# Kernel tuning notes

Hardware: AMD Instinct MI355X
Metric: run time of the kernel (lower is better)

The kernel has to match this reference:

```python
import jax, jax.numpy as jnp
import numpy as np
from jax import lax

B, C, T = 8, 512, 2048
TEMP = 0.07
EPS = 1e-12


def setup_inputs() -> dict:
    key = jax.random.key(0)
    k1, k2, k3, k4 = jax.random.split(key, 4)
    x = jax.random.normal(k1, (B, C, T), dtype=jnp.float32)
    w_qkv = jax.random.normal(k2, (3 * C, C, 1), dtype=jnp.float32) * (1.0 / np.sqrt(C))
    w_dw = jax.random.normal(k3, (3 * C, 1, 3), dtype=jnp.float32) * (1.0 / np.sqrt(3))
    w_proj = jax.random.normal(k4, (C, C, 1), dtype=jnp.float32) * (1.0 / np.sqrt(C))
    return {"x": x, "w_qkv": w_qkv, "w_dw": w_dw, "w_proj": w_proj}


def _l2norm_ch(a):
    # F.normalize(a, dim=1): divide by L2 norm over channel dim, clamped at eps
    n = jnp.sqrt(jnp.sum(a * a, axis=1, keepdims=True))
    return a / jnp.maximum(n, EPS)


def reference(x, w_qkv, w_dw, w_proj):
    # 1x1 conv: [B,C,T] x [3C,C] -> [B,3C,T]
    qkv = jnp.einsum('bct,oc->bot', x, w_qkv[:, :, 0])
    # depthwise conv, kernel 3, padding 1, groups = 3C
    qkv = lax.conv_general_dilated(
        qkv, w_dw, window_strides=(1,), padding=[(1, 1)],
        dimension_numbers=('NCH', 'OIH', 'NCH'), feature_group_count=3 * C)
    q, k, v = jnp.split(qkv, 3, axis=1)  # each [B,C,T]
    q = _l2norm_ch(q)
    k = _l2norm_ch(k)
    # attn over tokens: [B,T,T]
    attn = jax.nn.softmax(jnp.einsum('bct,bcs->bts', q, k) / TEMP, axis=-1)
    out = jnp.einsum('bts,bcs->bct', attn, v)  # [B,C,T]
    return jnp.einsum('bct,oc->bot', out, w_proj[:, :, 0])
```

## Files before the change

### kernel.cpp

```cpp
#include <hip/hip_runtime.h>
#include <math.h>

static constexpr int B_ = 8, C_ = 512, T_ = 2048, C3_ = 1536;
static constexpr float INV_TEMP = 1.0f / 0.07f;

typedef __attribute__((ext_vector_type(8))) short short8;
typedef __attribute__((ext_vector_type(4))) float floatx4;

__device__ __forceinline__ float b2f(unsigned short u) {
  union { unsigned int i; float f; } v; v.i = ((unsigned int)u) << 16; return v.f;
}
__device__ __forceinline__ unsigned short f2b(float f) {
  union { float f; unsigned int i; } v; v.f = f;
  const unsigned int x = v.i;
  return (unsigned short)((x + 0x7FFFu + ((x >> 16) & 1u)) >> 16);
}
__device__ __forceinline__ void gld16(const unsigned short* g, unsigned short* l) {
  __builtin_amdgcn_global_load_lds(
      (const __attribute__((address_space(1))) void*)g,
      (__attribute__((address_space(3))) void*)l, 16, 0, 0);
}

#define FENCE  asm volatile("" ::: "memory")
#define BAR()  do { FENCE; __builtin_amdgcn_s_barrier(); FENCE; } while (0)
#define LGKM0  asm volatile("s_waitcnt lgkmcnt(0)" ::: "memory")
#define VMC4   asm volatile("s_waitcnt vmcnt(4)" ::: "memory")
#define VMC0   asm volatile("s_waitcnt vmcnt(0)" ::: "memory")

template<bool OUT_BF16, int MODE>
__global__ __launch_bounds__(512, 2)
void gemm256(const unsigned short* __restrict__ A, const unsigned short* __restrict__ B,
             void* __restrict__ Cout, int K, int lda, int ldb, int ldc,
             long long sA, long long sB, long long sC,
             const float* __restrict__ rs, const float* __restrict__ cs,
             float* __restrict__ denom, int rcStride, float scale)
{
  extern __shared__ unsigned short S[];

  const int bz = blockIdx.z;
  A += (long long)bz * sA;
  B += (long long)bz * sB;
  if (MODE == 2) { rs += (long long)bz * rcStride; cs += (long long)bz * rcStride;
                   denom += (long long)bz * rcStride; }
  if (MODE == 3) { rs += (long long)bz * rcStride; }
  const int m0 = blockIdx.y * 256, n0 = blockIdx.x * 256;
  const int tid = threadIdx.x;
  const int w = tid >> 6, lane = tid & 63;
  const int rl = lane & 15, qd = lane >> 4;
  const int wm = (w >> 2) * 128, wn = (w & 3) * 64;

  const int lr = lane >> 3;
  const int lg = ((lane & 7) ^ lr) * 8;
  const unsigned short* gA = A + (long long)(m0 + w * 8 + lr) * lda + lg;
  const unsigned short* gB = B + (long long)(n0 + w * 8 + lr) * ldb + lg;

  const int g0 = (qd ^ (rl & 7)) * 8;
  const int g1 = ((4 + qd) ^ (rl & 7)) * 8;
  const int aBase = (wm + rl) * 64, bBase = (wn + rl) * 64;

  floatx4 acc[8][4];
  #pragma unroll
  for (int i = 0; i < 8; ++i)
    #pragma unroll
    for (int j = 0; j < 4; ++j) acc[i][j] = 0.0f;

  auto stA = [&](int buf, int h, int kt) {
    unsigned short* d = S + buf * 32768 + h * 8192 + w * 512;
    const unsigned short* s = gA + (long long)(h * 128) * lda + kt * 64;
    gld16(s, d);
    gld16(s + (long long)64 * lda, d + 4096);
  };
  auto stB = [&](int buf, int h, int kt) {
    unsigned short* d = S + buf * 32768 + 16384 + h * 8192 + w * 512;
    const unsigned short* s = gB + (long long)(h * 128) * ldb + kt * 64;
    gld16(s, d);
    gld16(s + (long long)64 * ldb, d + 4096);
  };

  short8 fa[4][2], fl[2][2], fr[2][2];
  auto rdA = [&](int buf, int ih) {
    const unsigned short* p = S + buf * 32768 + aBase + ih * 4096;
    #pragma unroll
    for (int i = 0; i < 4; ++i) {
      fa[i][0] = *(const short8*)(p + i * 1024 + g0);
      fa[i][1] = *(const short8*)(p + i * 1024 + g1);
    }
  };
  auto rdB = [&](short8 (&fb)[2][2], int buf, int jh) {
    const unsigned short* p = S + buf * 32768 + 16384 + bBase + jh * 2048;
    #pragma unroll
    for (int j = 0; j < 2; ++j) {
      fb[j][0] = *(const short8*)(p + j * 1024 + g0);
      fb[j][1] = *(const short8*)(p + j * 1024 + g1);
    }
  };
  auto mm = [&](short8 (&fb)[2][2], int ih, int jh) {
    #pragma unroll
    for (int i = 0; i < 4; ++i)
      #pragma unroll
      for (int j = 0; j < 2; ++j) {
        floatx4& a = acc[ih * 4 + i][jh * 2 + j];
        a = __builtin_amdgcn_mfma_f32_16x16x32_bf16(fa[i][0], fb[j][0], a, 0, 0, 0);
        a = __builtin_amdgcn_mfma_f32_16x16x32_bf16(fa[i][1], fb[j][1], a, 0, 0, 0);
      }
  };

  auto iter = [&](int kt, bool st2, bool st3, bool tail) {
    rdA(0, 0); rdB(fl, 0, 0);
    stA(1, 0, kt + 1);
    BAR(); LGKM0;
    __builtin_amdgcn_s_setprio(1); mm(fl, 0, 0); __builtin_amdgcn_s_setprio(0);
    BAR();
    rdB(fr, 0, 1);
    stA(1, 1, kt + 1);
    BAR(); LGKM0;
    __builtin_amdgcn_s_setprio(1); mm(fr, 0, 1); __builtin_amdgcn_s_setprio(0);
    BAR();
    rdA(0, 1);
    if (st2) stB(0, 0, kt + 2);
    BAR(); LGKM0;
    __builtin_amdgcn_s_setprio(1); mm(fl, 1, 0); __builtin_amdgcn_s_setprio(0);
    BAR();
    if (st2) stB(0, 1, kt + 2);
    if (tail) { VMC0; } else { VMC4; }
    BAR();
    __builtin_amdgcn_s_setprio(1); mm(fr, 1, 1); __builtin_amdgcn_s_setprio(0);
    BAR();
    rdA(1, 0); rdB(fl, 1, 0);
    if (st2) stA(0, 0, kt + 2);
    BAR(); LGKM0;
    __builtin_amdgcn_s_setprio(1); mm(fl, 0, 0); __builtin_amdgcn_s_setprio(0);
    BAR();
    rdB(fr, 1, 1);
    if (st2) stA(0, 1, kt + 2);
    BAR(); LGKM0;
    __builtin_amdgcn_s_setprio(1); mm(fr, 0, 1); __builtin_amdgcn_s_setprio(0);
    BAR();
    rdA(1, 1);
    if (st3) stB(1, 0, kt + 3);
    BAR(); LGKM0;
    __builtin_amdgcn_s_setprio(1); mm(fl, 1, 0); __builtin_amdgcn_s_setprio(0);
    BAR();
    if (st3) stB(1, 1, kt + 3);
    if (!tail) { VMC4; }
    BAR();
    __builtin_amdgcn_s_setprio(1); mm(fr, 1, 1); __builtin_amdgcn_s_setprio(0);
    BAR();
  };

  const int niter = K >> 7;
  stB(0, 0, 0); stB(0, 1, 0); stA(0, 0, 0); stA(0, 1, 0);
  stB(1, 0, 1); stB(1, 1, 1);
  VMC4; BAR();
  for (int i = 0; i < niter - 1; ++i) iter(2 * i, true, true, false);
  iter(2 * (niter - 1), false, false, true);

  float cf4[4];
  if (MODE == 2) {
    #pragma unroll
    for (int j = 0; j < 4; ++j) cf4[j] = cs[n0 + wn + j * 16 + rl];
  }
  #pragma unroll
  for (int i = 0; i < 8; ++i) {
    #pragma unroll
    for (int r = 0; r < 4; ++r) {
      const int row = m0 + wm + i * 16 + qd * 4 + r;
      float rowf = 0.f;
      if (MODE == 2) rowf = rs[row] * scale;
      if (MODE == 3) rowf = 1.0f / rs[row];
      float rsum = 0.f;
      #pragma unroll
      for (int j = 0; j < 4; ++j) {
        const int col = n0 + wn + j * 16 + rl;
        float v = acc[i][j][r];
        if (MODE == 2) {
          const float s = v * rowf * cf4[j];
          const unsigned short pb = f2b(__expf(s - scale));
          rsum += b2f(pb);
          ((unsigned short*)Cout)[(long long)bz * sC + (long long)row * ldc + col] = pb;
          continue;
        }
        if (MODE == 3) v *= rowf;
        const long long idx = (long long)bz * sC + (long long)row * ldc + col;
        if (OUT_BF16) ((unsigned short*)Cout)[idx] = f2b(v);
        else          ((float*)Cout)[idx] = v;
      }
      if (MODE == 2) {
        #pragma unroll
        for (int m = 1; m < 16; m <<= 1) rsum += __shfl_xor(rsum, m);
        if (rl == 0) atomicAdd(denom + row, rsum);
      }
    }
  }
}

__global__ __launch_bounds__(256)
void zero_f(float* __restrict__ p, int n)
{
  const int i = blockIdx.x * 256 + threadIdx.x;
  if (i < n) p[i] = 0.f;
}

__global__ __launch_bounds__(256)
void conv_xT(const float* __restrict__ x, unsigned short* __restrict__ xT)
{
  const int b = blockIdx.z, t0 = blockIdx.x * 32, c0 = blockIdx.y * 32;
  const int tx = threadIdx.x & 31, ty = threadIdx.x >> 5;
  __shared__ float tile[32][33];
  const float* src = x + (long long)b * C_ * T_;
  #pragma unroll
  for (int r = 0; r < 4; ++r)
    tile[ty + 8 * r][tx] = src[(long long)(c0 + ty + 8 * r) * T_ + t0 + tx];
  __syncthreads();
  unsigned short* dst = xT + (long long)b * T_ * C_;
  #pragma unroll
  for (int r = 0; r < 4; ++r)
    dst[(long long)(t0 + ty + 8 * r) * C_ + c0 + tx] = f2b(tile[tx][ty + 8 * r]);
}

__global__ __launch_bounds__(256)
void conv_bf(const float* __restrict__ in, unsigned short* __restrict__ out, int n)
{
  const int i = blockIdx.x * 256 + threadIdx.x;
  if (i < n) out[i] = f2b(in[i]);
}

__global__ __launch_bounds__(256)
void dw_v(const unsigned short* __restrict__ qkv, const float* __restrict__ wdw,
          unsigned short* __restrict__ vout)
{
  const long long idx = (long long)blockIdx.x * 256 + threadIdx.x;
  const int t = (int)(idx % T_);
  const long long rem = idx / T_;
  const int c = (int)(rem % C_), b = (int)(rem / C_);
  const unsigned short* src = qkv + ((long long)(b * C3_ + 2 * C_ + c)) * T_;
  const float* wp = wdw + (2 * C_ + c) * 3;
  const float xm = (t > 0)      ? b2f(src[t - 1]) : 0.f;
  const float x0 = b2f(src[t]);
  const float xp = (t < T_ - 1) ? b2f(src[t + 1]) : 0.f;
  vout[(long long)(b * C_ + c) * T_ + t] = f2b(fmaf(wp[0], xm, fmaf(wp[1], x0, wp[2] * xp)));
}

__global__ __launch_bounds__(256)
void dw_qk_t(const unsigned short* __restrict__ qkv, const float* __restrict__ wdw,
             unsigned short* __restrict__ qT, unsigned short* __restrict__ kT)
{
  const int bz = blockIdx.z, b = bz >> 1, p = bz & 1;
  const int t0 = blockIdx.x * 32, c0 = blockIdx.y * 32;
  const int tx = threadIdx.x & 31, ty = threadIdx.x >> 5;
  __shared__ float tin[32][34];
  __shared__ float tout[32][33];
  const int chb = b * C3_ + p * C_;
  #pragma unroll
  for (int r = 0; r < 4; ++r) {
    const int cy = ty + 8 * r;
    const unsigned short* src = qkv + (long long)(chb + c0 + cy) * T_;
    int t = t0 - 1 + tx;
    tin[cy][tx] = (t >= 0 && t < T_) ? b2f(src[t]) : 0.f;
    if (tx < 2) {
      const int t2 = t0 + 31 + tx;
      tin[cy][32 + tx] = (t2 < T_) ? b2f(src[t2]) : 0.f;
    }
  }
  __syncthreads();
  #pragma unroll
  for (int r = 0; r < 4; ++r) {
    const int cy = ty + 8 * r;
    const float* wp = wdw + (long long)(p * C_ + c0 + cy) * 3;
    tout[tx][cy] = fmaf(wp[0], tin[cy][tx], fmaf(wp[1], tin[cy][tx + 1], wp[2] * tin[cy][tx + 2]));
  }
  __syncthreads();
  unsigned short* dst = (p == 0 ? qT : kT) + (long long)b * T_ * C_;
  #pragma unroll
  for (int r = 0; r < 4; ++r)
    dst[(long long)(t0 + ty + 8 * r) * C_ + c0 + tx] = f2b(tout[ty + 8 * r][tx]);
}

__global__ __launch_bounds__(256)
void norms_k(const unsigned short* __restrict__ qT, const unsigned short* __restrict__ kT,
             float* __restrict__ inv_nq, float* __restrict__ inv_nk)
{
  const int wave = threadIdx.x >> 6, lane = threadIdx.x & 63;
  const long long row = (long long)blockIdx.x * 4 + wave;
  const unsigned short* src = (blockIdx.y == 0 ? qT : kT) + row * C_ + lane * 8;
  const uint4 u = *(const uint4*)src;
  float ss = 0.f;
  const unsigned int uu[4] = {u.x, u.y, u.z, u.w};
  #pragma unroll
  for (int i = 0; i < 4; ++i) {
    const float lo = b2f(uu[i] & 0xFFFF), hi = b2f(uu[i] >> 16);
    ss = fmaf(lo, lo, ss); ss = fmaf(hi, hi, ss);
  }
  #pragma unroll
  for (int m = 32; m; m >>= 1) ss += __shfl_xor(ss, m);
  if (lane == 0)
    (blockIdx.y == 0 ? inv_nq : inv_nk)[row] = 1.f / fmaxf(sqrtf(ss), 1e-12f);
}

extern "C" void kernel_launch(void* const* d_in, const int* in_sizes, int n_in,
                              void* d_out, int out_size, void* d_ws, size_t ws_size,
                              hipStream_t stream)
{
  const float* x      = (const float*)d_in[0];
  const float* w_qkv  = (const float*)d_in[1];
  const float* w_dw   = (const float*)d_in[2];
  const float* w_proj = (const float*)d_in[3];
  float* out = (float*)d_out;

  static int attr_done = 0;
  if (!attr_done) {
    hipFuncSetAttribute((const void*)&gemm256<true, 0>,
                        hipFuncAttributeMaxDynamicSharedMemorySize, 131072);
    hipFuncSetAttribute((const void*)&gemm256<true, 2>,
                        hipFuncAttributeMaxDynamicSharedMemorySize, 131072);
    hipFuncSetAttribute((const void*)&gemm256<true, 3>,
                        hipFuncAttributeMaxDynamicSharedMemorySize, 131072);
    hipFuncSetAttribute((const void*)&gemm256<false, 0>,
                        hipFuncAttributeMaxDynamicSharedMemorySize, 131072);
    attr_done = 1;
  }

  char* base = (char*)d_ws;
  unsigned short* xT      = (unsigned short*)base;
  unsigned short* wqkv_bf = (unsigned short*)(base + 16777216);
  unsigned short* av_t    = (unsigned short*)base;
  char* p = base + 67108864;
  unsigned short* qT = (unsigned short*)p; p += 16777216;
  unsigned short* kT = (unsigned short*)p; p += 16777216;
  unsigned short* vb = (unsigned short*)p; p += 16777216;
  unsigned short* attn   = (unsigned short*)p;
  unsigned short* qkv_bf = (unsigned short*)p;
  p += 67108864;
  unsigned short* wproj_bf = (unsigned short*)p; p += 524288;
  float* inv_nq = (float*)p; p += 65536;
  float* inv_nk = (float*)p; p += 65536;
  float* denom  = (float*)p;

  const long long TC = (long long)T_ * C_, TT = (long long)T_ * T_;

  conv_xT<<<dim3(T_ / 32, C_ / 32, B_), 256, 0, stream>>>(x, xT);
  conv_bf<<<(C3_ * C_) / 256, 256, 0, stream>>>(w_qkv, wqkv_bf, C3_ * C_);
  conv_bf<<<(C_ * C_) / 256, 256, 0, stream>>>(w_proj, wproj_bf, C_ * C_);
  zero_f<<<(B_ * T_) / 256, 256, 0, stream>>>(denom, B_ * T_);

  gemm256<true, 0><<<dim3(8, 6, B_), 512, 131072, stream>>>(
      wqkv_bf, xT, qkv_bf, C_, C_, C_, T_,
      0LL, TC, (long long)C3_ * T_, nullptr, nullptr, nullptr, 0, 1.f);

  dw_v<<<(int)(((long long)B_ * C_ * T_) / 256), 256, 0, stream>>>(qkv_bf, w_dw, vb);
  dw_qk_t<<<dim3(T_ / 32, C_ / 32, B_ * 2), 256, 0, stream>>>(qkv_bf, w_dw, qT, kT);

  norms_k<<<dim3((B_ * T_) / 4, 2), 256, 0, stream>>>(qT, kT, inv_nq, inv_nk);

  gemm256<true, 2><<<dim3(8, 8, B_), 512, 131072, stream>>>(
      qT, kT, attn, C_, C_, C_, T_,
      TC, TC, TT, inv_nq, inv_nk, denom, T_, INV_TEMP);

  gemm256<true, 3><<<dim3(2, 8, B_), 512, 131072, stream>>>(
      attn, vb, av_t, T_, T_, T_, C_,
      TT, (long long)C_ * T_, TC, denom, nullptr, nullptr, T_, 1.f);

  gemm256<false, 0><<<dim3(8, 2, B_), 512, 131072, stream>>>(
      wproj_bf, av_t, out, C_, C_, C_, T_,
      0LL, TC, (long long)C_ * T_, nullptr, nullptr, nullptr, 0, 1.f);
}
```

Baseline: 340.9 us.

## Add 128x128 triple-buffered GEMM for smaller matmuls and retune 256-tile pipeline

Adds a new 128x128-tile, 256-thread GEMM kernel with a three-stage global-to-LDS pipeline and uses it for the QKV projection, attn·V, and output projection, which had too few 256x256 tiles to fill the GPU (e.g. 128 blocks for attn·V). The large 256-tile kernel stays only for the QK^T scores GEMM. That kernel gets sched_barrier fences and moves one A-tile prefetch earlier, with a matching vmcnt(6) wait. The smaller tiles give more blocks for occupancy but less data reuse per block.

```diff
diff --git a/kernel.cpp b/kernel.cpp
--- a/kernel.cpp
+++ b/kernel.cpp
@@ -24,8 +24,128 @@
 #define FENCE  asm volatile("" ::: "memory")
 #define BAR()  do { FENCE; __builtin_amdgcn_s_barrier(); FENCE; } while (0)
 #define LGKM0  asm volatile("s_waitcnt lgkmcnt(0)" ::: "memory")
+#define VMC6   asm volatile("s_waitcnt vmcnt(6)" ::: "memory")
 #define VMC4   asm volatile("s_waitcnt vmcnt(4)" ::: "memory")
 #define VMC0   asm volatile("s_waitcnt vmcnt(0)" ::: "memory")
+#define SCHED0 __builtin_amdgcn_sched_barrier(0)
+
+template<bool OUT_BF16, int MODE>
+__global__ __launch_bounds__(256)
+void gemm_tn(const unsigned short* __restrict__ A, const unsigned short* __restrict__ B,
+             void* __restrict__ Cout, int K, int lda, int ldb, int ldc,
+             long long sA, long long sB, long long sC,
+             const float* __restrict__ rs, const float* __restrict__ cs,
+             float* __restrict__ denom, int rcStride, float scale)
+{
+  constexpr int NL = 4;
+
+  const int bz = blockIdx.z;
+  A += (long long)bz * sA;
+  B += (long long)bz * sB;
+  if (MODE == 2) { rs += (long long)bz * rcStride; cs += (long long)bz * rcStride;
+                   denom += (long long)bz * rcStride; }
+  if (MODE == 3) { rs += (long long)bz * rcStride; }
+  const int m0 = blockIdx.y * 128, n0 = blockIdx.x * 128;
+  const int tid = threadIdx.x;
+  const int w = tid >> 6, lane = tid & 63;
+  const int wm = (w >> 1) * 64, wn = (w & 1) * 64;
+  const int rl = lane & 15, qd = lane >> 4;
+
+  __shared__ __align__(16) unsigned short As[3][128 * 32];
+  __shared__ __align__(16) unsigned short Bs[3][128 * 32];
+
+  const int sr = lane >> 2, sg = lane & 3;
+  const int ml0 = 32 * w + sr, ml1 = ml0 + 16;
+  const int q0 = sg ^ ((ml0 >> 1) & 3), q1 = sg ^ ((ml1 >> 1) & 3);
+  const unsigned short* gA0 = A + (long long)(m0 + ml0) * lda + q0 * 8;
+  const unsigned short* gA1 = A + (long long)(m0 + ml1) * lda + q1 * 8;
+  const unsigned short* gB0 = B + (long long)(n0 + ml0) * ldb + q0 * 8;
+  const unsigned short* gB1 = B + (long long)(n0 + ml1) * ldb + q1 * 8;
+
+  int aoff[4], boff[4];
+  #pragma unroll
+  for (int i = 0; i < 4; ++i) {
+    const int mr = wm + i * 16 + rl;
+    aoff[i] = mr * 32 + ((qd ^ ((mr >> 1) & 3)) * 8);
+    const int nr = wn + i * 16 + rl;
+    boff[i] = nr * 32 + ((qd ^ ((nr >> 1) & 3)) * 8);
+  }
+
+  floatx4 acc[4][4];
+  #pragma unroll
+  for (int i = 0; i < 4; ++i)
+    #pragma unroll
+    for (int j = 0; j < 4; ++j) acc[i][j] = 0.0f;
+
+  auto stage = [&](int t, int bf) {
+    const int ko = t * 32;
+    gld16(gA0 + ko, As[bf] + (32 * w) * 32);
+    gld16(gA1 + ko, As[bf] + (32 * w + 16) * 32);
+    gld16(gB0 + ko, Bs[bf] + (32 * w) * 32);
+    gld16(gB1 + ko, Bs[bf] + (32 * w + 16) * 32);
+  };
+  auto compute = [&](int bf) {
+    short8 fa[4], fb[4];
+    #pragma unroll
+    for (int i = 0; i < 4; ++i) fa[i] = *(const short8*)(As[bf] + aoff[i]);
+    #pragma unroll
+    for (int j = 0; j < 4; ++j) fb[j] = *(const short8*)(Bs[bf] + boff[j]);
+    #pragma unroll
+    for (int i = 0; i < 4; ++i)
+      #pragma unroll
+      for (int j = 0; j < 4; ++j)
+        acc[i][j] = __builtin_amdgcn_mfma_f32_16x16x32_bf16(fa[i], fb[j], acc[i][j], 0, 0, 0);
+  };
+
+  const int niter = K >> 5;
+  stage(0, 0);
+  stage(1, 1);
+  int buf = 0;
+  for (int i = 0; i < niter - 1; ++i) {
+    asm volatile("s_waitcnt vmcnt(%0)\n\ts_barrier" :: "i"(NL) : "memory");
+    if (i + 2 < niter) {
+      int nb = buf + 2; if (nb >= 3) nb -= 3;
+      stage(i + 2, nb);
+    }
+    compute(buf);
+    if (++buf == 3) buf = 0;
+  }
+  asm volatile("s_waitcnt vmcnt(0)\n\ts_barrier" ::: "memory");
+  compute(buf);
+
+  #pragma unroll
+  for (int i = 0; i < 4; ++i) {
+    #pragma unroll
+    for (int r = 0; r < 4; ++r) {
+      const int row = m0 + wm + i * 16 + qd * 4 + r;
+      float rowf = 0.f;
+      if (MODE == 2) rowf = rs[row] * scale;
+      if (MODE == 3) rowf = 1.0f / rs[row];
+      float rsum = 0.f;
+      #pragma unroll
+      for (int j = 0; j < 4; ++j) {
+        const int col = n0 + wn + j * 16 + rl;
+        float v = acc[i][j][r];
+        if (MODE == 2) {
+          const float s = v * rowf * cs[col];
+          const unsigned short pb = f2b(__expf(s - scale));
+          rsum += b2f(pb);
+          ((unsigned short*)Cout)[(long long)bz * sC + (long long)row * ldc + col] = pb;
+          continue;
+        }
+        if (MODE == 3) v *= rowf;
+        const long long idx = (long long)bz * sC + (long long)row * ldc + col;
+        if (OUT_BF16) ((unsigned short*)Cout)[idx] = f2b(v);
+        else          ((float*)Cout)[idx] = v;
+      }
+      if (MODE == 2) {
+        #pragma unroll
+        for (int m = 1; m < 16; m <<= 1) rsum += __shfl_xor(rsum, m);
+        if (rl == 0) atomicAdd(denom + row, rsum);
+      }
+    }
+  }
+}
 
 template<bool OUT_BF16, int MODE>
 __global__ __launch_bounds__(512, 2)
@@ -108,42 +228,41 @@
   auto iter = [&](int kt, bool st2, bool st3, bool tail) {
     rdA(0, 0); rdB(fl, 0, 0);
     stA(1, 0, kt + 1);
-    BAR(); LGKM0;
+    BAR(); LGKM0; SCHED0;
     __builtin_amdgcn_s_setprio(1); mm(fl, 0, 0); __builtin_amdgcn_s_setprio(0);
     BAR();
     rdB(fr, 0, 1);
     stA(1, 1, kt + 1);
-    BAR(); LGKM0;
+    BAR(); LGKM0; SCHED0;
     __builtin_amdgcn_s_setprio(1); mm(fr, 0, 1); __builtin_amdgcn_s_setprio(0);
     BAR();
     rdA(0, 1);
     if (st2) stB(0, 0, kt + 2);
-    BAR(); LGKM0;
+    BAR(); LGKM0; SCHED0;
     __builtin_amdgcn_s_setprio(1); mm(fl, 1, 0); __builtin_amdgcn_s_setprio(0);
     BAR();
-    if (st2) stB(0, 1, kt + 2);
-    if (tail) { VMC0; } else { VMC4; }
-    BAR();
+    if (st2) { stB(0, 1, kt + 2); stA(0, 0, kt + 2); }
+    if (tail) { VMC0; } else { VMC6; }
+    BAR(); SCHED0;
     __builtin_amdgcn_s_setprio(1); mm(fr, 1, 1); __builtin_amdgcn_s_setprio(0);
     BAR();
     rdA(1, 0); rdB(fl, 1, 0);
-    if (st2) stA(0, 0, kt + 2);
-    BAR(); LGKM0;
+    if (st2) stA(0, 1, kt + 2);
+    BAR(); LGKM0; SCHED0;
     __builtin_amdgcn_s_setprio(1); mm(fl, 0, 0); __builtin_amdgcn_s_setprio(0);
     BAR();
     rdB(fr, 1, 1);
-    if (st2) stA(0, 1, kt + 2);
-    BAR(); LGKM0;
+    BAR(); LGKM0; SCHED0;
     __builtin_amdgcn_s_setprio(1); mm(fr, 0, 1); __builtin_amdgcn_s_setprio(0);
     BAR();
     rdA(1, 1);
     if (st3) stB(1, 0, kt + 3);
-    BAR(); LGKM0;
+    BAR(); LGKM0; SCHED0;
     __builtin_amdgcn_s_setprio(1); mm(fl, 1, 0); __builtin_amdgcn_s_setprio(0);
     BAR();
     if (st3) stB(1, 1, kt + 3);
     if (!tail) { VMC4; }
-    BAR();
+    BAR(); SCHED0;
     __builtin_amdgcn_s_setprio(1); mm(fr, 1, 1); __builtin_amdgcn_s_setprio(0);
     BAR();
   };
@@ -309,13 +428,7 @@
 
   static int attr_done = 0;
   if (!attr_done) {
-    hipFuncSetAttribute((const void*)&gemm256<true, 0>,
-                        hipFuncAttributeMaxDynamicSharedMemorySize, 131072);
     hipFuncSetAttribute((const void*)&gemm256<true, 2>,
-                        hipFuncAttributeMaxDynamicSharedMemorySize, 131072);
-    hipFuncSetAttribute((const void*)&gemm256<true, 3>,
-                        hipFuncAttributeMaxDynamicSharedMemorySize, 131072);
-    hipFuncSetAttribute((const void*)&gemm256<false, 0>,
                         hipFuncAttributeMaxDynamicSharedMemorySize, 131072);
     attr_done = 1;
   }
@@ -343,7 +456,7 @@
   conv_bf<<<(C_ * C_) / 256, 256, 0, stream>>>(w_proj, wproj_bf, C_ * C_);
   zero_f<<<(B_ * T_) / 256, 256, 0, stream>>>(denom, B_ * T_);
 
-  gemm256<true, 0><<<dim3(8, 6, B_), 512, 131072, stream>>>(
+  gemm_tn<true, 0><<<dim3(16, 12, B_), 256, 0, stream>>>(
       wqkv_bf, xT, qkv_bf, C_, C_, C_, T_,
       0LL, TC, (long long)C3_ * T_, nullptr, nullptr, nullptr, 0, 1.f);
 
@@ -356,11 +469,11 @@
       qT, kT, attn, C_, C_, C_, T_,
       TC, TC, TT, inv_nq, inv_nk, denom, T_, INV_TEMP);
 
-  gemm256<true, 3><<<dim3(2, 8, B_), 512, 131072, stream>>>(
+  gemm_tn<true, 3><<<dim3(4, 16, B_), 256, 0, stream>>>(
       attn, vb, av_t, T_, T_, T_, C_,
       TT, (long long)C_ * T_, TC, denom, nullptr, nullptr, T_, 1.f);
 
-  gemm256<false, 0><<<dim3(8, 2, B_), 512, 131072, stream>>>(
+  gemm_tn<false, 0><<<dim3(16, 4, B_), 256, 0, stream>>>(
       wproj_bf, av_t, out, C_, C_, C_, T_,
       0LL, TC, (long long)C_ * T_, nullptr, nullptr, nullptr, 0, 1.f);
 }
```

Result: faster. 330.3 us (-3.1%).
